# Kernel tuning notes

Hardware: AMD Instinct MI355X
Metric: run time of the kernel (lower is better)

The kernel has to match this reference:

```python
import jax, jax.numpy as jnp
import numpy as np

D = 1024; NH = 16; HD = D // NH; B = 2; L = 2048
BASE_FAST = (1.0 + 5.0 ** 0.5) / 2.0
BASE_SLOW = 1618.0
BASE_GLU = 16180.0
ALPHA_ATTN = 0.42; ALPHA_MLP = 1.07; ALPHA_ADV = 1.0
H_GATE = max(8, D // 4)   # rope_gate hidden
H_NU = max(4, D // 8)     # DuplexViscosity hidden
LN_EPS = 1e-5


def _rope_cos_sin(seq_len, dim, base, dtype=jnp.float32):
    idx = jnp.arange(0, dim, 2, dtype=dtype) / float(dim)
    inv = 1.0 / (base ** idx)
    t = jnp.arange(seq_len, dtype=dtype)
    freqs = jnp.outer(t, inv)                       # (L, D/2)
    emb = jnp.concatenate([freqs, freqs], axis=-1)  # (L, D)
    return jnp.cos(emb)[None], jnp.sin(emb)[None]   # (1, L, D)


def _rotate_half(x):
    x1, x2 = jnp.split(x, 2, axis=-1)
    return jnp.concatenate([-x2, x1], axis=-1)


def _apply_rope(x, cos, sin):
    return x * cos + _rotate_half(x) * sin


def setup_inputs() -> dict:
    key = jax.random.key(0)
    ks = jax.random.split(key, 16)
    std = 0.02
    # all Linear weights stored as (in, out) so forward is x @ W + b
    return {
        "z": jax.random.normal(ks[0], (B, L, D), jnp.float32),
        "Wq": jax.random.normal(ks[1], (D, D), jnp.float32) * std,
        "bq": jnp.zeros((D,), jnp.float32),
        "Wk": jax.random.normal(ks[2], (D, D), jnp.float32) * std,
        "bk": jnp.zeros((D,), jnp.float32),
        "Wv": jax.random.normal(ks[3], (D, D), jnp.float32) * std,
        "bv": jnp.zeros((D,), jnp.float32),
        "Wcoh": jax.random.normal(ks[4], (D, D), jnp.float32) * std,
        "gamma": jnp.zeros((1,), jnp.float32),
        "rg_w1": jax.random.normal(ks[5], (D, H_GATE), jnp.float32) * std,
        "rg_b1": jnp.zeros((H_GATE,), jnp.float32),
        "rg_w2": jax.random.normal(ks[6], (H_GATE, 1), jnp.float32) * std,
        "rg_b2": jnp.zeros((1,), jnp.float32),
        "nu_diff": jnp.asarray(0.2, jnp.float32),
        "nu_adv": jnp.asarray(0.01, jnp.float32),
        "nu_w1": jax.random.normal(ks[7], (D, H_NU), jnp.float32) * std,
        "nu_b1": jnp.zeros((H_NU,), jnp.float32),
        "nu_w2": jax.random.normal(ks[8], (H_NU, 1), jnp.float32) * std,
        "nu_b2": jnp.zeros((1,), jnp.float32),
        "Wu": jax.random.normal(ks[9], (D, D), jnp.float32) * std,
        "bu": jnp.zeros((D,), jnp.float32),
        "Wg": jax.random.normal(ks[10], (D, D), jnp.float32) * std,
        "bg": jnp.zeros((D,), jnp.float32),
        "ln_w": jnp.ones((D,), jnp.float32),
        "ln_b": jnp.zeros((D,), jnp.float32),
        "Cw": jax.random.normal(ks[11], (D, D), jnp.float32) * std,
        "Cb": jnp.zeros((D,), jnp.float32),
    }


def reference(z, Wq, bq, Wk, bk, Wv, bv, Wcoh, gamma, rg_w1, rg_b1, rg_w2, rg_b2,
              nu_diff, nu_adv, nu_w1, nu_b1, nu_w2, nu_b2, Wu, bu, Wg, bg,
              ln_w, ln_b, Cw, Cb):
    b, l, d = z.shape
    dt = z.dtype
    # causal cumulative mean pool[t] = mean(z[0..t])
    pool = jnp.cumsum(z, axis=1) / jnp.arange(1, l + 1, dtype=dt)[None, :, None]

    # QKV projections
    Q = z @ Wq + bq
    K_raw = z @ Wk + bk
    V = z @ Wv + bv

    # global coherence bias: (B, Lq, Lk)
    gk = pool @ Wcoh
    gb = jnp.einsum('bld,bmd->blm', gk, K_raw) * (d ** -0.5)
    gb = jnp.tanh(gamma[0]) * gb

    # hybrid RoPE gate (small MLP on pool, exact gelu as in torch)
    gate = jax.nn.sigmoid(jax.nn.gelu(pool @ rg_w1 + rg_b1, approximate=False) @ rg_w2 + rg_b2)  # (B,L,1)
    cos_f, sin_f = _rope_cos_sin(l, d, BASE_FAST, dt)
    cos_s, sin_s = _rope_cos_sin(l, d, BASE_SLOW, dt)
    cos = gate * cos_f + (1.0 - gate) * cos_s
    sin = gate * sin_f + (1.0 - gate) * sin_s
    Qr = _apply_rope(Q, cos, sin)
    Kr = _apply_rope(K_raw, cos, sin)

    # multi-head causal attention with fused coherence bias
    Qh = Qr.reshape(b, l, NH, HD).transpose(0, 2, 1, 3)
    Kh = Kr.reshape(b, l, NH, HD).transpose(0, 2, 1, 3)
    Vh = V.reshape(b, l, NH, HD).transpose(0, 2, 1, 3)
    logits = jnp.einsum('bhld,bhmd->bhlm', Qh, Kh) * (HD ** -0.5)
    logits = logits + gb[:, None]
    causal = jnp.tril(jnp.ones((l, l), bool))
    logits = jnp.where(causal[None, None], logits, -jnp.inf)
    attn = jax.nn.softmax(logits, axis=-1)
    attn_out = jnp.einsum('bhlm,bhmd->bhld', attn, Vh).transpose(0, 2, 1, 3).reshape(b, l, d)
    attn_w = attn.mean(axis=1)

    # DuplexViscosity on causal pool
    delta = jnp.tanh(jnp.tanh(pool @ nu_w1 + nu_b1) @ nu_w2 + nu_b2) * jnp.abs(nu_adv)
    nu_b = jnp.abs(nu_diff) + delta  # (B,L,1)

    # GLU branch with fixed slow-base RoPE
    cos_g, sin_g = _rope_cos_sin(l, d, BASE_GLU, dt)
    z_glu = _apply_rope(z, cos_g, sin_g)
    bilinear = (z_glu @ Wu + bu) * (z_glu @ Wg + bg)
    adv = -(ALPHA_ADV * nu_b) * bilinear
    mu = adv.mean(axis=-1, keepdims=True)
    var = ((adv - mu) ** 2).mean(axis=-1, keepdims=True)
    adv_n = (adv - mu) * jax.lax.rsqrt(var + LN_EPS) * ln_w + ln_b
    mlp_out = adv_n @ Cw + Cb

    z_next = z + ALPHA_ATTN * attn_out + ALPHA_MLP * mlp_out
    return z_next, attn_w
```

## Files before the change

kernel.cpp:

```cpp
#include <hip/hip_runtime.h>

#define DD 1024
#define NHH 16
#define HDD 64
#define BB 2
#define LL 2048
#define MM (BB*LL)
#define HG 256
#define HN 128

#define LOG_FAST 0.48121182f
#define LOG_SLOW 7.3889461f
#define LOG_GLU  9.6915312f
#define SCL 0.18033688f

typedef __attribute__((ext_vector_type(8))) short short8;
typedef __attribute__((ext_vector_type(4))) float f32x4;

__device__ __forceinline__ float gelu_f(float x) {
    return 0.5f * x * (1.0f + erff(x * 0.70710678f));
}

__device__ __forceinline__ ushort f2b(float x) {
    unsigned u = __float_as_uint(x);
    unsigned r = (u + 0x7FFFu + ((u >> 16) & 1u)) >> 16;
    return (ushort)r;
}

__device__ __forceinline__ float b2f(ushort x) {
    return __uint_as_float(((unsigned)x) << 16);
}

__device__ __forceinline__ void gl_lds16(const ushort* g, ushort* l) {
    __builtin_amdgcn_global_load_lds(
        (const __attribute__((address_space(1))) unsigned int*)g,
        (__attribute__((address_space(3))) unsigned int*)l, 16, 0, 0);
}

#define SWZC(row, c8) (((((row) << 3) | ((c8) ^ ((row) & 7)))) << 3)

__device__ __forceinline__ void stage_tile(const ushort* gsrc, int rstride,
                                           ushort* lds, int tid) {
    int wid = tid >> 6;
#pragma unroll
    for (int r = 0; r < 2; ++r) {
        int c = r * 256 + tid;
        int row = c >> 3;
        int c8 = (c & 7) ^ (row & 7);
        gl_lds16(gsrc + (size_t)row * rstride + c8 * 8,
                 lds + (size_t)(r * 256 + wid * 64) * 8);
    }
}

#define LCH 128
#define NCH 16
__global__ void pool_scan1(const float* __restrict__ z, float* __restrict__ part,
                           float* __restrict__ ctot, ushort* __restrict__ zb) {
    int ch = blockIdx.x, dg = blockIdx.y, b = blockIdx.z;
    int d = dg * 256 + threadIdx.x;
    size_t base = ((size_t)b * LL + ch * LCH) * DD + d;
    const float* zp = z + base;
    float* pp = part + base;
    ushort* zo = zb + base;
    float s = 0.f;
    for (int t = 0; t < LCH; ++t) {
        float v = zp[(size_t)t * DD];
        s += v;
        pp[(size_t)t * DD] = s;
        zo[(size_t)t * DD] = f2b(v);
    }
    ctot[((size_t)b * NCH + ch) * DD + d] = s;
}
__global__ void pool_scan2(const float* __restrict__ part, const float* __restrict__ ctot,
                           ushort* __restrict__ poolb) {
    int ch = blockIdx.x, dg = blockIdx.y, b = blockIdx.z;
    int d = dg * 256 + threadIdx.x;
    float off = 0.f;
    for (int c = 0; c < ch; ++c) off += ctot[((size_t)b * NCH + c) * DD + d];
    int t0 = ch * LCH;
    size_t base = ((size_t)b * LL + t0) * DD + d;
    const float* pp = part + base;
    ushort* po = poolb + base;
    for (int t = 0; t < LCH; ++t) {
        po[(size_t)t * DD] = f2b((pp[(size_t)t * DD] + off) / (float)(t0 + t + 1));
    }
}

__global__ void f2bT4_kernel(const float* __restrict__ W0, const float* __restrict__ W1,
                             const float* __restrict__ W2, const float* __restrict__ W3,
                             ushort* __restrict__ Wt) {
    const float* W = blockIdx.z == 0 ? W0 : (blockIdx.z == 1 ? W1 :
                     (blockIdx.z == 2 ? W2 : W3));
    ushort* dst = Wt + (size_t)blockIdx.z * 1024 * 1024;
    __shared__ float t[32][33];
    int n0 = blockIdx.x * 32, k0 = blockIdx.y * 32;
    int tx = threadIdx.x & 31, ty = threadIdx.x >> 5;
#pragma unroll
    for (int j = 0; j < 4; ++j)
        t[ty + j * 8][tx] = W[(size_t)(k0 + ty + j * 8) * 1024 + n0 + tx];
    __syncthreads();
#pragma unroll
    for (int j = 0; j < 4; ++j)
        dst[(size_t)(n0 + ty + j * 8) * 1024 + k0 + tx] = f2b(t[tx][ty + j * 8]);
}

__global__ void f2bT_rgnu(const float* __restrict__ Wrg, const float* __restrict__ Wnu,
                          ushort* __restrict__ WtRG, ushort* __restrict__ WtNU) {
    int zc = blockIdx.z;
    if (zc == 1 && blockIdx.x >= 4) return;
    const float* W = zc == 0 ? Wrg : Wnu;
    ushort* dst = zc == 0 ? WtRG : WtNU;
    int Ndim = zc == 0 ? HG : HN;
    __shared__ float t[32][33];
    int n0 = blockIdx.x * 32, k0 = blockIdx.y * 32;
    int tx = threadIdx.x & 31, ty = threadIdx.x >> 5;
#pragma unroll
    for (int j = 0; j < 4; ++j)
        t[ty + j * 8][tx] = W[(size_t)(k0 + ty + j * 8) * Ndim + n0 + tx];
    __syncthreads();
#pragma unroll
    for (int j = 0; j < 4; ++j)
        dst[(size_t)(n0 + ty + j * 8) * 1024 + k0 + tx] = f2b(t[tx][ty + j * 8]);
}

__global__ void f2bT3_kernel(const float* __restrict__ W0, const float* __restrict__ W1,
                             const float* __restrict__ W2, ushort* __restrict__ Wt) {
    const float* W = blockIdx.z == 0 ? W0 : (blockIdx.z == 1 ? W1 : W2);
    ushort* dst = Wt + (size_t)blockIdx.z * 1024 * 1024;
    __shared__ float t[32][33];
    int n0 = blockIdx.x * 32, k0 = blockIdx.y * 32;
    int tx = threadIdx.x & 31, ty = threadIdx.x >> 5;
#pragma unroll
    for (int j = 0; j < 4; ++j)
        t[ty + j * 8][tx] = W[(size_t)(k0 + ty + j * 8) * 1024 + n0 + tx];
    __syncthreads();
#pragma unroll
    for (int j = 0; j < 4; ++j)
        dst[(size_t)(n0 + ty + j * 8) * 1024 + k0 + tx] = f2b(t[tx][ty + j * 8]);
}

__global__ __launch_bounds__(256) void gemm_mfma(
        const ushort* __restrict__ A, const ushort* __restrict__ Wt,
        const float* __restrict__ bias, float* __restrict__ C, int Ndim) {
    __shared__ ushort As[4096];
    __shared__ ushort Bs[4096];
    int tid = threadIdx.x;
    int wid = tid >> 6, lane = tid & 63;
    int n0 = blockIdx.x * 128, m0 = blockIdx.y * 128;
    int wm = wid >> 1, wn = wid & 1;
    int quad = lane >> 4, l16 = lane & 15;

    f32x4 acc[4][4];
#pragma unroll
    for (int mi = 0; mi < 4; ++mi)
#pragma unroll
        for (int ni = 0; ni < 4; ++ni) acc[mi][ni] = (f32x4){0.f, 0.f, 0.f, 0.f};

    int c0 = wid * 128 + lane;
    int c1 = c0 + 64;
    const ushort* Ag0 = A + (size_t)(m0 + (c0 & 127)) * 1024 + (c0 >> 7) * 8;
    const ushort* Ag1 = A + (size_t)(m0 + (c1 & 127)) * 1024 + (c1 >> 7) * 8;
    const ushort* Bg0 = Wt + (size_t)(n0 + (c0 & 127)) * 1024 + (c0 >> 7) * 8;
    const ushort* Bg1 = Wt + (size_t)(n0 + (c1 & 127)) * 1024 + (c1 >> 7) * 8;
    ushort* Al0 = As + wid * 1024;
    ushort* Al1 = As + wid * 1024 + 512;
    ushort* Bl0 = Bs + wid * 1024;
    ushort* Bl1 = Bs + wid * 1024 + 512;

    const ushort* a_rd = &As[(quad * 128 + wm * 64 + l16) * 8];
    const ushort* b_rd = &Bs[(quad * 128 + wn * 64 + l16) * 8];

    for (int kb = 0; kb < 1024; kb += 32) {
        gl_lds16(Ag0 + kb, Al0);
        gl_lds16(Ag1 + kb, Al1);
        gl_lds16(Bg0 + kb, Bl0);
        gl_lds16(Bg1 + kb, Bl1);
        __syncthreads();
        short8 af[4], bf[4];
#pragma unroll
        for (int mi = 0; mi < 4; ++mi)
            af[mi] = *(const short8*)(a_rd + mi * 16 * 8);
#pragma unroll
        for (int ni = 0; ni < 4; ++ni)
            bf[ni] = *(const short8*)(b_rd + ni * 16 * 8);
#pragma unroll
        for (int mi = 0; mi < 4; ++mi)
#pragma unroll
            for (int ni = 0; ni < 4; ++ni)
                acc[mi][ni] = __builtin_amdgcn_mfma_f32_16x16x32_bf16(
                    af[mi], bf[ni], acc[mi][ni], 0, 0, 0);
        __syncthreads();
    }
    int bcol[4];
    float bval[4];
#pragma unroll
    for (int ni = 0; ni < 4; ++ni) {
        bcol[ni] = n0 + wn * 64 + ni * 16 + l16;
        bval[ni] = bias ? bias[bcol[ni]] : 0.f;
    }
#pragma unroll
    for (int mi = 0; mi < 4; ++mi) {
#pragma unroll
        for (int r = 0; r < 4; ++r) {
            int row = m0 + wm * 64 + mi * 16 + quad * 4 + r;
            float* Cp = C + (size_t)row * Ndim;
#pragma unroll
            for (int ni = 0; ni < 4; ++ni)
                Cp[bcol[ni]] = acc[mi][ni][r] + bval[ni];
        }
    }
}

__global__ __launch_bounds__(256) void gemm_mfma3(
        const ushort* __restrict__ A, const ushort* __restrict__ Wt,
        const float* __restrict__ b0, const float* __restrict__ b1,
        const float* __restrict__ b2, float* __restrict__ C,
        ushort* __restrict__ K16r) {
    int zid = blockIdx.z;
    const ushort* W = Wt + (size_t)zid * 1024 * 1024;
    const float* bias = zid == 0 ? b0 : (zid == 1 ? b1 : b2);
    float* Cz = C + (size_t)zid * (size_t)MM * DD;
    __shared__ ushort As[4096];
    __shared__ ushort Bs[4096];
    int tid = threadIdx.x;
    int wid = tid >> 6, lane = tid & 63;
    int n0 = blockIdx.x * 128, m0 = blockIdx.y * 128;
    int wm = wid >> 1, wn = wid & 1;
    int quad = lane >> 4, l16 = lane & 15;

    f32x4 acc[4][4];
#pragma unroll
    for (int mi = 0; mi < 4; ++mi)
#pragma unroll
        for (int ni = 0; ni < 4; ++ni) acc[mi][ni] = (f32x4){0.f, 0.f, 0.f, 0.f};

    int c0 = wid * 128 + lane;
    int c1 = c0 + 64;
    const ushort* Ag0 = A + (size_t)(m0 + (c0 & 127)) * 1024 + (c0 >> 7) * 8;
    const ushort* Ag1 = A + (size_t)(m0 + (c1 & 127)) * 1024 + (c1 >> 7) * 8;
    const ushort* Bg0 = W + (size_t)(n0 + (c0 & 127)) * 1024 + (c0 >> 7) * 8;
    const ushort* Bg1 = W + (size_t)(n0 + (c1 & 127)) * 1024 + (c1 >> 7) * 8;
    ushort* Al0 = As + wid * 1024;
    ushort* Al1 = As + wid * 1024 + 512;
    ushort* Bl0 = Bs + wid * 1024;
    ushort* Bl1 = Bs + wid * 1024 + 512;

    const ushort* a_rd = &As[(quad * 128 + wm * 64 + l16) * 8];
    const ushort* b_rd = &Bs[(quad * 128 + wn * 64 + l16) * 8];

    for (int kb = 0; kb < 1024; kb += 32) {
        gl_lds16(Ag0 + kb, Al0);
        gl_lds16(Ag1 + kb, Al1);
        gl_lds16(Bg0 + kb, Bl0);
        gl_lds16(Bg1 + kb, Bl1);
        __syncthreads();
        short8 af[4], bf[4];
#pragma unroll
        for (int mi = 0; mi < 4; ++mi)
            af[mi] = *(const short8*)(a_rd + mi * 16 * 8);
#pragma unroll
        for (int ni = 0; ni < 4; ++ni)
            bf[ni] = *(const short8*)(b_rd + ni * 16 * 8);
#pragma unroll
        for (int mi = 0; mi < 4; ++mi)
#pragma unroll
            for (int ni = 0; ni < 4; ++ni)
                acc[mi][ni] = __builtin_amdgcn_mfma_f32_16x16x32_bf16(
                    af[mi], bf[ni], acc[mi][ni], 0, 0, 0);
        __syncthreads();
    }
    float bval[4];
    int bcol[4];
#pragma unroll
    for (int ni = 0; ni < 4; ++ni) {
        bcol[ni] = n0 + wn * 64 + ni * 16 + l16;
        bval[ni] = bias[bcol[ni]];
    }
    bool doK = (zid == 1) && (K16r != nullptr);
#pragma unroll
    for (int mi = 0; mi < 4; ++mi) {
#pragma unroll
        for (int r = 0; r < 4; ++r) {
            int row = m0 + wm * 64 + mi * 16 + quad * 4 + r;
            float* Cp = Cz + (size_t)row * 1024;
            ushort* Kp = K16r + (size_t)row * 1024;
#pragma unroll
            for (int ni = 0; ni < 4; ++ni) {
                float v = acc[mi][ni][r] + bval[ni];
                Cp[bcol[ni]] = v;
                if (doK) Kp[bcol[ni]] = f2b(v);
            }
        }
    }
}

__global__ __launch_bounds__(256) void gemm_mfma_b16out(
        const ushort* __restrict__ A, const ushort* __restrict__ Wt,
        ushort* __restrict__ C, int Ndim) {
    __shared__ ushort As[4096];
    __shared__ ushort Bs[4096];
    int tid = threadIdx.x;
    int wid = tid >> 6, lane = tid & 63;
    int n0 = blockIdx.x * 128, m0 = blockIdx.y * 128;
    int wm = wid >> 1, wn = wid & 1;
    int quad = lane >> 4, l16 = lane & 15;

    f32x4 acc[4][4];
#pragma unroll
    for (int mi = 0; mi < 4; ++mi)
#pragma unroll
        for (int ni = 0; ni < 4; ++ni) acc[mi][ni] = (f32x4){0.f, 0.f, 0.f, 0.f};

    int c0 = wid * 128 + lane;
    int c1 = c0 + 64;
    const ushort* Ag0 = A + (size_t)(m0 + (c0 & 127)) * 1024 + (c0 >> 7) * 8;
    const ushort* Ag1 = A + (size_t)(m0 + (c1 & 127)) * 1024 + (c1 >> 7) * 8;
    const ushort* Bg0 = Wt + (size_t)(n0 + (c0 & 127)) * 1024 + (c0 >> 7) * 8;
    const ushort* Bg1 = Wt + (size_t)(n0 + (c1 & 127)) * 1024 + (c1 >> 7) * 8;
    ushort* Al0 = As + wid * 1024;
    ushort* Al1 = As + wid * 1024 + 512;
    ushort* Bl0 = Bs + wid * 1024;
    ushort* Bl1 = Bs + wid * 1024 + 512;

    const ushort* a_rd = &As[(quad * 128 + wm * 64 + l16) * 8];
    const ushort* b_rd = &Bs[(quad * 128 + wn * 64 + l16) * 8];

    for (int kb = 0; kb < 1024; kb += 32) {
        gl_lds16(Ag0 + kb, Al0);
        gl_lds16(Ag1 + kb, Al1);
        gl_lds16(Bg0 + kb, Bl0);
        gl_lds16(Bg1 + kb, Bl1);
        __syncthreads();
        short8 af[4], bf[4];
#pragma unroll
        for (int mi = 0; mi < 4; ++mi)
            af[mi] = *(const short8*)(a_rd + mi * 16 * 8);
#pragma unroll
        for (int ni = 0; ni < 4; ++ni)
            bf[ni] = *(const short8*)(b_rd + ni * 16 * 8);
#pragma unroll
        for (int mi = 0; mi < 4; ++mi)
#pragma unroll
            for (int ni = 0; ni < 4; ++ni)
                acc[mi][ni] = __builtin_amdgcn_mfma_f32_16x16x32_bf16(
                    af[mi], bf[ni], acc[mi][ni], 0, 0, 0);
        __syncthreads();
    }
#pragma unroll
    for (int mi = 0; mi < 4; ++mi) {
#pragma unroll
        for (int r = 0; r < 4; ++r) {
            int row = m0 + wm * 64 + mi * 16 + quad * 4 + r;
            ushort* Cp = C + (size_t)row * Ndim;
#pragma unroll
            for (int ni = 0; ni < 4; ++ni)
                Cp[n0 + wn * 64 + ni * 16 + l16] = f2b(acc[mi][ni][r]);
        }
    }
}

__global__ __launch_bounds__(256) void gemm_gates(
        const ushort* __restrict__ A, const ushort* __restrict__ WtRG,
        const ushort* __restrict__ WtNU, const float* __restrict__ rg_b1,
        const float* __restrict__ nu_b1, float* __restrict__ H1,
        float* __restrict__ N1) {
    int bx = blockIdx.x;
    bool isH = bx < 2;
    const ushort* Wt = isH ? WtRG : WtNU;
    const float* bias = isH ? rg_b1 : nu_b1;
    float* C = isH ? H1 : N1;
    int Ndim = isH ? HG : HN;
    int n0 = isH ? bx * 128 : 0;
    int m0 = blockIdx.y * 128;
    __shared__ ushort As[4096];
    __shared__ ushort Bs[4096];
    int tid = threadIdx.x;
    int wid = tid >> 6, lane = tid & 63;
    int wm = wid >> 1, wn = wid & 1;
    int quad = lane >> 4, l16 = lane & 15;

    f32x4 acc[4][4];
#pragma unroll
    for (int mi = 0; mi < 4; ++mi)
#pragma unroll
        for (int ni = 0; ni < 4; ++ni) acc[mi][ni] = (f32x4){0.f, 0.f, 0.f, 0.f};

    int c0 = wid * 128 + lane;
    int c1 = c0 + 64;
    const ushort* Ag0 = A + (size_t)(m0 + (c0 & 127)) * 1024 + (c0 >> 7) * 8;
    const ushort* Ag1 = A + (size_t)(m0 + (c1 & 127)) * 1024 + (c1 >> 7) * 8;
    const ushort* Bg0 = Wt + (size_t)(n0 + (c0 & 127)) * 1024 + (c0 >> 7) * 8;
    const ushort* Bg1 = Wt + (size_t)(n0 + (c1 & 127)) * 1024 + (c1 >> 7) * 8;
    ushort* Al0 = As + wid * 1024;
    ushort* Al1 = As + wid * 1024 + 512;
    ushort* Bl0 = Bs + wid * 1024;
    ushort* Bl1 = Bs + wid * 1024 + 512;

    const ushort* a_rd = &As[(quad * 128 + wm * 64 + l16) * 8];
    const ushort* b_rd = &Bs[(quad * 128 + wn * 64 + l16) * 8];

    for (int kb = 0; kb < 1024; kb += 32) {
        gl_lds16(Ag0 + kb, Al0);
        gl_lds16(Ag1 + kb, Al1);
        gl_lds16(Bg0 + kb, Bl0);
        gl_lds16(Bg1 + kb, Bl1);
        __syncthreads();
        short8 af[4], bf[4];
#pragma unroll
        for (int mi = 0; mi < 4; ++mi)
            af[mi] = *(const short8*)(a_rd + mi * 16 * 8);
#pragma unroll
        for (int ni = 0; ni < 4; ++ni)
            bf[ni] = *(const short8*)(b_rd + ni * 16 * 8);
#pragma unroll
        for (int mi = 0; mi < 4; ++mi)
#pragma unroll
            for (int ni = 0; ni < 4; ++ni)
                acc[mi][ni] = __builtin_amdgcn_mfma_f32_16x16x32_bf16(
                    af[mi], bf[ni], acc[mi][ni], 0, 0, 0);
        __syncthreads();
    }
    int bcol[4];
    float bval[4];
#pragma unroll
    for (int ni = 0; ni < 4; ++ni) {
        bcol[ni] = n0 + wn * 64 + ni * 16 + l16;
        bval[ni] = bias[bcol[ni]];
    }
#pragma unroll
    for (int mi = 0; mi < 4; ++mi) {
#pragma unroll
        for (int r = 0; r < 4; ++r) {
            int row = m0 + wm * 64 + mi * 16 + quad * 4 + r;
            float* Cp = C + (size_t)row * Ndim;
#pragma unroll
            for (int ni = 0; ni < 4; ++ni)
                Cp[bcol[ni]] = acc[mi][ni][r] + bval[ni];
        }
    }
}

__global__ __launch_bounds__(256) void gb_mfma(
        const ushort* __restrict__ gk16, const ushort* __restrict__ K16r,
        const float* __restrict__ gamma, ushort* __restrict__ gb) {
    int lt = blockIdx.x >> 4, mt = blockIdx.x & 15;
    if (mt > lt) return;
    int b = blockIdx.y;
    __shared__ ushort As[4096];
    __shared__ ushort Bs[4096];
    int tid = threadIdx.x;
    int wid = tid >> 6, lane = tid & 63;
    int l0 = lt * 128, m0 = mt * 128;
    int wm = wid >> 1, wn = wid & 1;
    int quad = lane >> 4, l16 = lane & 15;

    f32x4 acc[4][4];
#pragma unroll
    for (int mi = 0; mi < 4; ++mi)
#pragma unroll
        for (int ni = 0; ni < 4; ++ni) acc[mi][ni] = (f32x4){0.f, 0.f, 0.f, 0.f};

    int c0 = wid * 128 + lane;
    int c1 = c0 + 64;
    const ushort* Ag0 = gk16 + ((size_t)b * LL + l0 + (c0 & 127)) * 1024 + (c0 >> 7) * 8;
    const ushort* Ag1 = gk16 + ((size_t)b * LL + l0 + (c1 & 127)) * 1024 + (c1 >> 7) * 8;
    const ushort* Bg0 = K16r + ((size_t)b * LL + m0 + (c0 & 127)) * 1024 + (c0 >> 7) * 8;
    const ushort* Bg1 = K16r + ((size_t)b * LL + m0 + (c1 & 127)) * 1024 + (c1 >> 7) * 8;
    ushort* Al0 = As + wid * 1024;
    ushort* Al1 = As + wid * 1024 + 512;
    ushort* Bl0 = Bs + wid * 1024;
    ushort* Bl1 = Bs + wid * 1024 + 512;

    const ushort* a_rd = &As[(quad * 128 + wm * 64 + l16) * 8];
    const ushort* b_rd = &Bs[(quad * 128 + wn * 64 + l16) * 8];

    for (int kb = 0; kb < 1024; kb += 32) {
        gl_lds16(Ag0 + kb, Al0);
        gl_lds16(Ag1 + kb, Al1);
        gl_lds16(Bg0 + kb, Bl0);
        gl_lds16(Bg1 + kb, Bl1);
        __syncthreads();
        short8 af[4], bf[4];
#pragma unroll
        for (int mi = 0; mi < 4; ++mi)
            af[mi] = *(const short8*)(a_rd + mi * 16 * 8);
#pragma unroll
        for (int ni = 0; ni < 4; ++ni)
            bf[ni] = *(const short8*)(b_rd + ni * 16 * 8);
#pragma unroll
        for (int mi = 0; mi < 4; ++mi)
#pragma unroll
            for (int ni = 0; ni < 4; ++ni)
                acc[mi][ni] = __builtin_amdgcn_mfma_f32_16x16x32_bf16(
                    af[mi], bf[ni], acc[mi][ni], 0, 0, 0);
        __syncthreads();
    }
    float scale = tanhf(gamma[0]) * 0.25f;
#pragma unroll
    for (int mi = 0; mi < 4; ++mi) {
#pragma unroll
        for (int r = 0; r < 4; ++r) {
            int row = l0 + wm * 64 + mi * 16 + quad * 4 + r;
            ushort* Cp = gb + ((size_t)b * LL + row) * LL;
            ushort4 o;
            o.x = f2b(acc[mi][0][r] * scale);
            o.y = f2b(acc[mi][1][r] * scale);
            o.z = f2b(acc[mi][2][r] * scale);
            o.w = f2b(acc[mi][3][r] * scale);
            *(ushort4*)(Cp + m0 + wn * 64 + l16 * 4) = o;
        }
    }
}

__global__ __launch_bounds__(256) void gatenu_fin(
        const float* __restrict__ H1, const float* __restrict__ N1,
        const float* __restrict__ rg_w2, const float* __restrict__ rg_b2,
        const float* __restrict__ nu_w2, const float* __restrict__ nu_b2,
        const float* __restrict__ nu_diff, const float* __restrict__ nu_adv,
        float* __restrict__ gate, float* __restrict__ nub) {
    int row = blockIdx.x, tid = threadIdx.x;
    float gv = gelu_f(H1[(size_t)row * HG + tid]) * rg_w2[tid];
    float nv = (tid < HN) ? tanhf(N1[(size_t)row * HN + tid]) * nu_w2[tid] : 0.f;
    for (int off = 32; off; off >>= 1) {
        gv += __shfl_down(gv, off);
        nv += __shfl_down(nv, off);
    }
    __shared__ float pg[4], pn[4];
    if ((tid & 63) == 0) { pg[tid >> 6] = gv; pn[tid >> 6] = nv; }
    __syncthreads();
    if (tid == 0) {
        float ga = pg[0] + pg[1] + pg[2] + pg[3] + rg_b2[0];
        gate[row] = 1.f / (1.f + expf(-ga));
        float na = pn[0] + pn[1] + pn[2] + pn[3] + nu_b2[0];
        nub[row] = fabsf(nu_diff[0]) + tanhf(na) * fabsf(nu_adv[0]);
    }
}

__global__ void rope_qk_bf16(const float* __restrict__ Q, const float* __restrict__ K,
                             const float* __restrict__ gate,
                             ushort* __restrict__ Q16, ushort* __restrict__ K16) {
    int idx = blockIdx.x * 256 + threadIdx.x;
    int row = idx >> 9;
    int i = idx & 511;
    int b = row >> 11, t = row & (LL - 1);
    float g = gate[row];
    float fi = (float)i * (1.0f / 512.0f);
    float tf = (float)t;
    float af = tf * expf(-fi * LOG_FAST);
    float as = tf * expf(-fi * LOG_SLOW);
    float c = g * cosf(af) + (1.f - g) * cosf(as);
    float s = g * sinf(af) + (1.f - g) * sinf(as);
    size_t base = (size_t)row * DD;
    float x = Q[base + i], y = Q[base + 512 + i];
    float q1 = x * c - y * s, q2 = y * c + x * s;
    x = K[base + i]; y = K[base + 512 + i];
    float k1 = x * c - y * s, k2 = y * c + x * s;
    int h1 = i >> 6, d1 = i & 63;
    size_t o1 = ((size_t)(b * 16 + h1) * LL + t) * 64 + d1;
    size_t o2 = ((size_t)(b * 16 + 8 + h1) * LL + t) * 64 + d1;
    Q16[o1] = f2b(q1); Q16[o2] = f2b(q2);
    K16[o1] = f2b(k1); K16[o2] = f2b(k2);
}

__global__ __launch_bounds__(256) void vt16_kernel(const float* __restrict__ V,
                                                   ushort* __restrict__ VT) {
    __shared__ ushort t[64][72];
    int lb = blockIdx.x, hb = blockIdx.y, b = blockIdx.z;
    int tid = threadIdx.x;
    {
        int l = tid >> 2, c0 = (tid & 3) * 16;
        const float* Vp = V + ((size_t)(b * LL) + lb * 64 + l) * DD + hb * 64 + c0;
#pragma unroll
        for (int j = 0; j < 4; ++j) {
            float4 v = *(const float4*)(Vp + j * 4);
            t[l][c0 + j * 4 + 0] = f2b(v.x);
            t[l][c0 + j * 4 + 1] = f2b(v.y);
            t[l][c0 + j * 4 + 2] = f2b(v.z);
            t[l][c0 + j * 4 + 3] = f2b(v.w);
        }
    }
    __syncthreads();
    {
        int d = tid >> 2, l0 = (tid & 3) * 16;
        ushort tmp[16];
#pragma unroll
        for (int j = 0; j < 16; ++j) tmp[j] = t[l0 + j][d];
        ushort* Op = VT + ((size_t)((b * 16 + hb) * 64) + d) * LL + lb * 64 + l0;
        *(ushort4*)(Op + 0)  = *(ushort4*)&tmp[0];
        *(ushort4*)(Op + 4)  = *(ushort4*)&tmp[4];
        *(ushort4*)(Op + 8)  = *(ushort4*)&tmp[8];
        *(ushort4*)(Op + 12) = *(ushort4*)&tmp[12];
    }
}

__global__ void rope_glu_b16(const float* __restrict__ z, ushort* __restrict__ zg) {
    int idx = blockIdx.x * 256 + threadIdx.x;
    int row = idx >> 9;
    int i = idx & 511;
    int t = row & (LL - 1);
    float fi = (float)i * (1.0f / 512.0f);
    float ag = (float)t * expf(-fi * LOG_GLU);
    float c = cosf(ag), s = sinf(ag);
    size_t base = (size_t)row * DD;
    float x = z[base + i], y = z[base + 512 + i];
    zg[base + i]       = f2b(x * c - y * s);
    zg[base + 512 + i] = f2b(y * c + x * s);
}

__global__ __launch_bounds__(256, 4) void attn_flash_mfma(
        const ushort* __restrict__ Q16, const ushort* __restrict__ K16,
        const ushort* __restrict__ VT16, const ushort* __restrict__ gb16,
        float* __restrict__ attn_out, float* __restrict__ stats) {
    int h = blockIdx.x, qt = 31 - blockIdx.y, b = blockIdx.z;
    __shared__ ushort Ks0[4096];
    __shared__ ushort Vs0[4096];
    __shared__ ushort Ks1[4096];
    __shared__ ushort Vs1[4096];
    __shared__ ushort Ps[4096];
    int tid = threadIdx.x, wid = tid >> 6, lane = tid & 63;
    int quad = lane >> 4, l16 = lane & 15;
    const ushort* Qg = Q16 + ((size_t)(b * 16 + h) * LL) * 64;
    const ushort* Kg = K16 + ((size_t)(b * 16 + h) * LL) * 64;
    const ushort* Vg = VT16 + ((size_t)(b * 16 + h) * 64) * LL;
    const ushort* gbB = gb16 + (size_t)b * LL * LL;
    float* stB = stats + ((size_t)(b * 16 + h) * LL) * 2;
    int qrow = wid * 16 + quad * 4;
    int q0 = qt * 64;

    short8 qf[2];
    {
        const ushort* qp = Qg + (size_t)(q0 + wid * 16 + l16) * 64 + quad * 8;
        qf[0] = *(const short8*)(qp);
        qf[1] = *(const short8*)(qp + 32);
    }
    stage_tile(Kg, 64, Ks0, tid);
    stage_tile(Vg, LL, Vs0, tid);
    __syncthreads();

    ushort* Pw = Ps + wid * 1024;

    short ov = (l16 == 0) ? (short)0x3F80 : (short)0;
    short8 onesf = {ov, ov, ov, ov, ov, ov, ov, ov};

    f32x4 ofr[5];
    float m_r[4];
#pragma unroll
    for (int nt = 0; nt < 5; ++nt) ofr[nt] = (f32x4){0.f, 0.f, 0.f, 0.f};
#pragma unroll
    for (int r = 0; r < 4; ++r) m_r[r] = -3e38f;

#define FLASH_PHASE(KC, VC, KN, VN, T) do {                                       \
    int k0_ = (T) * 64;                                                           \
    ushort4 gw_[4];                                                               \
    _Pragma("unroll")                                                             \
    for (int r = 0; r < 4; ++r)                                                   \
        gw_[r] = *(const ushort4*)(gbB + (size_t)(q0 + qrow + r) * LL + k0_ + l16 * 4); \
    f32x4 sf_[4];                                                                 \
    _Pragma("unroll")                                                             \
    for (int nt = 0; nt < 4; ++nt) sf_[nt] = (f32x4){0.f, 0.f, 0.f, 0.f};         \
    _Pragma("unroll")                                                             \
    for (int ks = 0; ks < 2; ++ks)                                                \
        _Pragma("unroll")                                                         \
        for (int nt = 0; nt < 4; ++nt) {                                          \
            short8 kf_ = *(const short8*)((KC) + SWZC(nt * 16 + l16, ks * 4 + quad)); \
            sf_[nt] = __builtin_amdgcn_mfma_f32_16x16x32_bf16(qf[ks], kf_, sf_[nt], 0, 0, 0); \
        }                                                                         \
    short8 vf_[2][4];                                                             \
    _Pragma("unroll")                                                             \
    for (int ks = 0; ks < 2; ++ks)                                                \
        _Pragma("unroll")                                                         \
        for (int nt = 0; nt < 4; ++nt)                                            \
            vf_[ks][nt] = *(const short8*)((VC) + SWZC(nt * 16 + l16, ks * 4 + quad)); \
    if ((T) + 1 <= qt) {                                                          \
        stage_tile(Kg + (size_t)(k0_ + 64) * 64, 64, (KN), tid);                  \
        stage_tile(Vg + (k0_ + 64), LL, (VN), tid);                               \
    }                                                                             \
    _Pragma("unroll")                                                             \
    for (int r = 0; r < 4; ++r) {                                                 \
        sf_[0][r] += b2f(gw_[r].x); sf_[1][r] += b2f(gw_[r].y);                   \
        sf_[2][r] += b2f(gw_[r].z); sf_[3][r] += b2f(gw_[r].w);                   \
    }                                                                             \
    if ((T) == qt) {                                                              \
        _Pragma("unroll")                                                         \
        for (int nt = 0; nt < 4; ++nt)                                            \
            _Pragma("unroll")                                                     \
            for (int r = 0; r < 4; ++r)                                           \
                if (nt * 16 + l16 > qrow + r) sf_[nt][r] = -1e30f;                \
    }                                                                             \
    float alpha_[4], mS_[4];                                                      \
    _Pragma("unroll")                                                             \
    for (int r = 0; r < 4; ++r) {                                                 \
        float m_ = fmaxf(fmaxf(sf_[0][r], sf_[1][r]), fmaxf(sf_[2][r], sf_[3][r])); \
        _Pragma("unroll")                                                         \
        for (int off = 1; off < 16; off <<= 1)                                    \
            m_ = fmaxf(m_, __shfl_xor(m_, off));                                  \
        float nm_ = fmaxf(m_r[r], m_);                                            \
        alpha_[r] = __builtin_amdgcn_exp2f((m_r[r] - nm_) * SCL);                 \
        m_r[r] = nm_;                                                             \
        mS_[r] = nm_ * SCL;                                                       \
    }                                                                             \
    _Pragma("unroll")                                                             \
    for (int nt = 0; nt < 4; ++nt)                                                \
        _Pragma("unroll")                                                         \
        for (int r = 0; r < 4; ++r) {                                             \
            float p_ = __builtin_amdgcn_exp2f(fmaf(sf_[nt][r], SCL, -mS_[r]));    \
            int prow_ = quad * 4 + r;                                             \
            int chk_ = (nt * 2) | (l16 >> 3);                                     \
            Pw[prow_ * 64 + ((chk_ ^ (prow_ & 7)) << 3) + (l16 & 7)] = f2b(p_);   \
        }                                                                         \
    _Pragma("unroll")                                                             \
    for (int nt = 0; nt < 5; ++nt)                                                \
        _Pragma("unroll")                                                         \
        for (int r = 0; r < 4; ++r) ofr[nt][r] *= alpha_[r];                      \
    short8 pf_[2];                                                                \
    _Pragma("unroll")                                                             \
    for (int ks = 0; ks < 2; ++ks)                                                \
        pf_[ks] = *(const short8*)(Pw + l16 * 64 + (((ks * 4 + quad) ^ (l16 & 7)) << 3)); \
    __builtin_amdgcn_s_setprio(1);                                                \
    _Pragma("unroll")                                                             \
    for (int ks = 0; ks < 2; ++ks) {                                              \
        _Pragma("unroll")                                                         \
        for (int nt = 0; nt < 4; ++nt)                                            \
            ofr[nt] = __builtin_amdgcn_mfma_f32_16x16x32_bf16(pf_[ks], vf_[ks][nt], ofr[nt], 0, 0, 0); \
        ofr[4] = __builtin_amdgcn_mfma_f32_16x16x32_bf16(pf_[ks], onesf, ofr[4], 0, 0, 0); \
    }                                                                             \
    __builtin_amdgcn_s_setprio(0);                                                \
    __syncthreads();                                                              \
} while (0)

    for (int kt = 0; kt <= qt; kt += 2) {
        FLASH_PHASE(Ks0, Vs0, Ks1, Vs1, kt);
        if (kt + 1 <= qt) FLASH_PHASE(Ks1, Vs1, Ks0, Vs0, kt + 1);
    }
#undef FLASH_PHASE

#pragma unroll
    for (int r = 0; r < 4; ++r) {
        float l = __shfl(ofr[4][r], (lane & 48));
        float rinv = 1.0f / l;
        float* op = attn_out + ((size_t)(b * LL) + q0 + qrow + r) * DD + h * 64 + l16;
#pragma unroll
        for (int nt = 0; nt < 4; ++nt)
            op[nt * 16] = ofr[nt][r] * rinv;
    }
    if (l16 == 0) {
#pragma unroll
        for (int r = 0; r < 4; ++r) {
            size_t si = (size_t)(q0 + qrow + r) * 2;
            stB[si]     = m_r[r];
            stB[si + 1] = ofr[4][r];
        }
    }
}

__global__ __launch_bounds__(256, 4) void attn_w_mfma(
        const ushort* __restrict__ Q16, const ushort* __restrict__ K16,
        const ushort* __restrict__ gb16, const float* __restrict__ stats,
        float* __restrict__ aw) {
    int qt = blockIdx.x >> 5, kt = blockIdx.x & 31;
    int b = blockIdx.y;
    int tid = threadIdx.x, wid = tid >> 6, lane = tid & 63;
    int quad = lane >> 4, l16 = lane & 15;
    int q0 = qt * 64, k0 = kt * 64;
    int qrow = wid * 16 + quad * 4;
    if (kt > qt) {
        int rr = tid >> 2, c0 = (tid & 3) * 16;
        float4 zv = make_float4(0.f, 0.f, 0.f, 0.f);
        float* p = aw + ((size_t)(b * LL) + q0 + rr) * LL + k0 + c0;
#pragma unroll
        for (int j = 0; j < 4; ++j) *(float4*)(p + j * 4) = zv;
        return;
    }
    __shared__ ushort Qs0[4096];
    __shared__ ushort Ks0[4096];
    __shared__ ushort Qs1[4096];
    __shared__ ushort Ks1[4096];
    float acc[4][4];
#pragma unroll
    for (int nt = 0; nt < 4; ++nt)
#pragma unroll
        for (int r = 0; r < 4; ++r) acc[nt][r] = 0.f;
    f32x4 gacc[4];
    const ushort* gbB = gb16 + (size_t)b * LL * LL;
#pragma unroll
    for (int r = 0; r < 4; ++r) {
        ushort4 g4 = *(const ushort4*)(gbB + (size_t)(q0 + qrow + r) * LL + k0 + l16 * 4);
        gacc[0][r] = b2f(g4.x);
        gacc[1][r] = b2f(g4.y);
        gacc[2][r] = b2f(g4.z);
        gacc[3][r] = b2f(g4.w);
    }
    bool diag = (kt == qt);
    stage_tile(Q16 + ((size_t)(b * 16) * LL + q0) * 64, 64, Qs0, tid);
    stage_tile(K16 + ((size_t)(b * 16) * LL + k0) * 64, 64, Ks0, tid);
    __syncthreads();

#define AW_PHASE(QC, KC, QN, KN, H) do {                                          \
    short8 qf_[2], kf_[2][4];                                                     \
    _Pragma("unroll")                                                             \
    for (int ks = 0; ks < 2; ++ks)                                                \
        qf_[ks] = *(const short8*)((QC) + SWZC(wid * 16 + l16, ks * 4 + quad));   \
    _Pragma("unroll")                                                             \
    for (int ks = 0; ks < 2; ++ks)                                                \
        _Pragma("unroll")                                                         \
        for (int nt = 0; nt < 4; ++nt)                                            \
            kf_[ks][nt] = *(const short8*)((KC) + SWZC(nt * 16 + l16, ks * 4 + quad)); \
    if ((H) < 15) {                                                               \
        stage_tile(Q16 + ((size_t)(b * 16 + (H) + 1) * LL + q0) * 64, 64, (QN), tid); \
        stage_tile(K16 + ((size_t)(b * 16 + (H) + 1) * LL + k0) * 64, 64, (KN), tid); \
    }                                                                             \
    float mS_[4], li_[4];                                                         \
    {                                                                             \
        const float* sp_ = stats + ((size_t)(b * 16 + (H)) * LL + q0 + qrow) * 2; \
        _Pragma("unroll")                                                         \
        for (int r = 0; r < 4; ++r) {                                             \
            mS_[r] = sp_[r * 2] * SCL;                                            \
            li_[r] = 1.0f / sp_[r * 2 + 1];                                       \
        }                                                                         \
    }                                                                             \
    f32x4 sf_[4];                                                                 \
    _Pragma("unroll")                                                             \
    for (int nt = 0; nt < 4; ++nt) sf_[nt] = gacc[nt];                            \
    __builtin_amdgcn_s_setprio(1);                                                \
    _Pragma("unroll")                                                             \
    for (int ks = 0; ks < 2; ++ks)                                                \
        _Pragma("unroll")                                                         \
        for (int nt = 0; nt < 4; ++nt)                                            \
            sf_[nt] = __builtin_amdgcn_mfma_f32_16x16x32_bf16(qf_[ks], kf_[ks][nt], sf_[nt], 0, 0, 0); \
    __builtin_amdgcn_s_setprio(0);                                                \
    _Pragma("unroll")                                                             \
    for (int nt = 0; nt < 4; ++nt)                                                \
        _Pragma("unroll")                                                         \
        for (int r = 0; r < 4; ++r) {                                             \
            int row_ = qrow + r;                                                  \
            if (!diag || (nt * 16 + l16 <= row_))                                 \
                acc[nt][r] += __builtin_amdgcn_exp2f(fmaf(sf_[nt][r], SCL, -mS_[r])) * li_[r]; \
        }                                                                         \
    __syncthreads();                                                              \
} while (0)

    for (int h = 0; h < NHH; h += 2) {
        AW_PHASE(Qs0, Ks0, Qs1, Ks1, h);
        AW_PHASE(Qs1, Ks1, Qs0, Ks0, h + 1);
    }
#undef AW_PHASE

#pragma unroll
    for (int r = 0; r < 4; ++r) {
        float* op = aw + ((size_t)(b * LL) + q0 + qrow + r) * LL + k0 + l16;
#pragma unroll
        for (int nt = 0; nt < 4; ++nt)
            op[nt * 16] = acc[nt][r] * 0.0625f;
    }
}

__global__ __launch_bounds__(256) void adv_ln_kernel(
        const float* __restrict__ U, const float* __restrict__ G,
        const float* __restrict__ nub, const float* __restrict__ lnw,
        const float* __restrict__ lnb, ushort* __restrict__ out) {
    int row = blockIdx.x, tid = threadIdx.x;
    size_t base = (size_t)row * DD + tid * 4;
    float4 u4 = *(const float4*)&U[base];
    float4 g4 = *(const float4*)&G[base];
    float nu = nub[row];
    float a[4];
    a[0] = -nu * u4.x * g4.x;
    a[1] = -nu * u4.y * g4.y;
    a[2] = -nu * u4.z * g4.z;
    a[3] = -nu * u4.w * g4.w;
    float ts = a[0] + a[1] + a[2] + a[3];
    float tq = a[0] * a[0] + a[1] * a[1] + a[2] * a[2] + a[3] * a[3];
    for (int off = 32; off; off >>= 1) {
        ts += __shfl_down(ts, off);
        tq += __shfl_down(tq, off);
    }
    __shared__ float r1[4], r2[4];
    if ((tid & 63) == 0) { r1[tid >> 6] = ts; r2[tid >> 6] = tq; }
    __syncthreads();
    __shared__ float s_mu, s_rs;
    if (tid == 0) {
        float S  = r1[0] + r1[1] + r1[2] + r1[3];
        float Qq = r2[0] + r2[1] + r2[2] + r2[3];
        float mu = S * (1.0f / 1024.f);
        float var = Qq * (1.0f / 1024.f) - mu * mu;
        s_mu = mu;
        s_rs = rsqrtf(var + 1e-5f);
    }
    __syncthreads();
    float mu = s_mu, rs = s_rs;
    float4 w4 = *(const float4*)&lnw[tid * 4];
    float4 b4 = *(const float4*)&lnb[tid * 4];
    ushort4 ov;
    ov.x = f2b((a[0] - mu) * rs * w4.x + b4.x);
    ov.y = f2b((a[1] - mu) * rs * w4.y + b4.y);
    ov.z = f2b((a[2] - mu) * rs * w4.z + b4.z);
    ov.w = f2b((a[3] - mu) * rs * w4.w + b4.w);
    *(ushort4*)&out[base] = ov;
}

__global__ void final_kernel(const float* __restrict__ z, const float* __restrict__ ao,
                             const float* __restrict__ mlp, float* __restrict__ out) {
    size_t i = ((size_t)blockIdx.x * 256 + threadIdx.x) * 4;
    float4 z4 = *(const float4*)&z[i];
    float4 a4 = *(const float4*)&ao[i];
    float4 m4 = *(const float4*)&mlp[i];
    float4 o;
    o.x = z4.x + 0.42f * a4.x + 1.07f * m4.x;
    o.y = z4.y + 0.42f * a4.y + 1.07f * m4.y;
    o.z = z4.z + 0.42f * a4.z + 1.07f * m4.z;
    o.w = z4.w + 0.42f * a4.w + 1.07f * m4.w;
    *(float4*)&out[i] = o;
}

extern "C" void kernel_launch(void* const* d_in, const int* in_sizes, int n_in,
                              void* d_out, int out_size, void* d_ws, size_t ws_size,
                              hipStream_t stream) {
    const float* z       = (const float*)d_in[0];
    const float* Wq      = (const float*)d_in[1];
    const float* bq      = (const float*)d_in[2];
    const float* Wk      = (const float*)d_in[3];
    const float* bk      = (const float*)d_in[4];
    const float* Wv      = (const float*)d_in[5];
    const float* bv      = (const float*)d_in[6];
    const float* Wcoh    = (const float*)d_in[7];
    const float* gamma   = (const float*)d_in[8];
    const float* rg_w1   = (const float*)d_in[9];
    const float* rg_b1   = (const float*)d_in[10];
    const float* rg_w2   = (const float*)d_in[11];
    const float* rg_b2   = (const float*)d_in[12];
    const float* nu_diff = (const float*)d_in[13];
    const float* nu_adv  = (const float*)d_in[14];
    const float* nu_w1   = (const float*)d_in[15];
    const float* nu_b1   = (const float*)d_in[16];
    const float* nu_w2   = (const float*)d_in[17];
    const float* nu_b2   = (const float*)d_in[18];
    const float* Wu      = (const float*)d_in[19];
    const float* bu      = (const float*)d_in[20];
    const float* Wg      = (const float*)d_in[21];
    const float* bg      = (const float*)d_in[22];
    const float* ln_w    = (const float*)d_in[23];
    const float* ln_b    = (const float*)d_in[24];
    const float* Cw      = (const float*)d_in[25];
    const float* Cb      = (const float*)d_in[26];

    float* out_z  = (float*)d_out;
    float* out_aw = out_z + (size_t)MM * DD;

    float* ws = (float*)d_ws;
    const size_t MD = (size_t)MM * DD;
    float* pool  = ws;
    float* Qb    = ws + MD;
    float* Kb    = ws + 2 * MD;
    float* Vb    = ws + 3 * MD;
    float* gkb   = ws + 4 * MD;
    float* gbb   = ws + 5 * MD;
    float* H1    = ws + 7 * MD;
    float* N1    = H1 + (size_t)MM * HG;
    float* gate  = N1 + (size_t)MM * HN;
    float* nub   = gate + MM;
    float* stats = nub + MM;
    float* ctot  = stats + (size_t)BB * NHH * LL * 2;

    char* gbase  = (char*)gbb;
    ushort* Ab   = (ushort*)gbase;
    ushort* Wb   = (ushort*)(gbase + (size_t)8 * 1024 * 1024);
    ushort* gb16 = (ushort*)(gbase + (size_t)16 * 1024 * 1024);
    ushort* WtRG = Wb;
    ushort* WtNU = Wb + (size_t)1024 * 1024;
    ushort* Q16  = (ushort*)Vb;
    ushort* K16  = (ushort*)Vb + MD;
    ushort* VT16 = (ushort*)pool;
    ushort* poolb = (ushort*)pool;
    float*  part = gkb;
    ushort* gk16 = (ushort*)gkb;
    ushort* K16r = (ushort*)gkb + MD;

    dim3 g128(8, 32);
    dim3 wT_g(32, 32);

    pool_scan1<<<dim3(NCH, 4, BB), 256, 0, stream>>>(z, part, ctot, Ab);
    pool_scan2<<<dim3(NCH, 4, BB), 256, 0, stream>>>(part, ctot, poolb);
    f2bT4_kernel<<<dim3(32, 32, 4), 256, 0, stream>>>(Wq, Wk, Wv, Wcoh, Wb);
    gemm_mfma3<<<dim3(8, 32, 3), 256, 0, stream>>>(Ab, Wb, bq, bk, bv, Qb, K16r);
    gemm_mfma_b16out<<<g128, 256, 0, stream>>>(poolb, Wb + (size_t)3 * 1024 * 1024, gk16, DD);
    f2bT_rgnu<<<dim3(8, 32, 2), 256, 0, stream>>>(rg_w1, nu_w1, WtRG, WtNU);
    gemm_gates<<<dim3(3, 32), 256, 0, stream>>>(poolb, WtRG, WtNU, rg_b1, nu_b1, H1, N1);
    gb_mfma<<<dim3(256, BB), 256, 0, stream>>>(gk16, K16r, gamma, gb16);
    gatenu_fin<<<dim3(MM), 256, 0, stream>>>(H1, N1, rg_w2, rg_b2, nu_w2, nu_b2,
                                             nu_diff, nu_adv, gate, nub);
    vt16_kernel<<<dim3(32, 16, BB), 256, 0, stream>>>(Vb, VT16);
    rope_qk_bf16<<<dim3((MM * 512) / 256), 256, 0, stream>>>(Qb, Kb, gate, Q16, K16);
    attn_flash_mfma<<<dim3(NHH, 32, BB), 256, 0, stream>>>(Q16, K16, VT16, gb16, gkb, stats);
    attn_w_mfma<<<dim3(1024, BB), 256, 0, stream>>>(Q16, K16, gb16, stats, out_aw);
    rope_glu_b16<<<dim3((MM * 512) / 256), 256, 0, stream>>>(z, Ab);
    f2bT3_kernel<<<dim3(32, 32, 3), 256, 0, stream>>>(Wu, Wg, Cw, Wb);
    gemm_mfma3<<<dim3(8, 32, 2), 256, 0, stream>>>(Ab, Wb, bu, bg, bg, Qb, nullptr);
    adv_ln_kernel<<<dim3(MM), 256, 0, stream>>>(Qb, Kb, nub, ln_w, ln_b, Ab);
    gemm_mfma<<<g128, 256, 0, stream>>>(Ab, Wb + (size_t)2 * 1024 * 1024, Cb, Qb, DD);
    final_kernel<<<dim3(MD / 4 / 256), 256, 0, stream>>>(z, gkb, Qb, out_z);
}
```

Measured before the change: 654.2 us.

## Pair causal query tiles per block and reorder fragment loads in attention

Each flash-attention block now handles two query tiles, qt and 31-qt, in sequence. This balances the causal workload across blocks and halves the grid, with launch bounds relaxed from 4 to 2 blocks per SM. The K/V prefetch is moved ahead of the QK MFMAs, the bias is loaded straight into the accumulators, and V and K fragments are read from LDS just before use instead of being preloaded. These changes cut register pressure and give the prefetch more time to complete, at the cost of fewer blocks in flight for latency hiding.

Measured after the change: 565.1 us. -13.6%, faster.

```diff
diff --git a/kernel.cpp b/kernel.cpp
--- a/kernel.cpp
+++ b/kernel.cpp
@@ -607,11 +607,11 @@
     zg[base + 512 + i] = f2b(y * c + x * s);
 }
 
-__global__ __launch_bounds__(256, 4) void attn_flash_mfma(
+__global__ __launch_bounds__(256, 2) void attn_flash_mfma(
         const ushort* __restrict__ Q16, const ushort* __restrict__ K16,
         const ushort* __restrict__ VT16, const ushort* __restrict__ gb16,
         float* __restrict__ attn_out, float* __restrict__ stats) {
-    int h = blockIdx.x, qt = 31 - blockIdx.y, b = blockIdx.z;
+    int h = blockIdx.x, b = blockIdx.z;
     __shared__ ushort Ks0[4096];
     __shared__ ushort Vs0[4096];
     __shared__ ushort Ks1[4096];
@@ -625,39 +625,24 @@
     const ushort* gbB = gb16 + (size_t)b * LL * LL;
     float* stB = stats + ((size_t)(b * 16 + h) * LL) * 2;
     int qrow = wid * 16 + quad * 4;
-    int q0 = qt * 64;
-
-    short8 qf[2];
-    {
-        const ushort* qp = Qg + (size_t)(q0 + wid * 16 + l16) * 64 + quad * 8;
-        qf[0] = *(const short8*)(qp);
-        qf[1] = *(const short8*)(qp + 32);
-    }
-    stage_tile(Kg, 64, Ks0, tid);
-    stage_tile(Vg, LL, Vs0, tid);
-    __syncthreads();
-
     ushort* Pw = Ps + wid * 1024;
 
     short ov = (l16 == 0) ? (short)0x3F80 : (short)0;
     short8 onesf = {ov, ov, ov, ov, ov, ov, ov, ov};
 
-    f32x4 ofr[5];
-    float m_r[4];
-#pragma unroll
-    for (int nt = 0; nt < 5; ++nt) ofr[nt] = (f32x4){0.f, 0.f, 0.f, 0.f};
-#pragma unroll
-    for (int r = 0; r < 4; ++r) m_r[r] = -3e38f;
-
 #define FLASH_PHASE(KC, VC, KN, VN, T) do {                                       \
     int k0_ = (T) * 64;                                                           \
-    ushort4 gw_[4];                                                               \
-    _Pragma("unroll")                                                             \
-    for (int r = 0; r < 4; ++r)                                                   \
-        gw_[r] = *(const ushort4*)(gbB + (size_t)(q0 + qrow + r) * LL + k0_ + l16 * 4); \
+    if ((T) + 1 <= qt) {                                                          \
+        stage_tile(Kg + (size_t)(k0_ + 64) * 64, 64, (KN), tid);                  \
+        stage_tile(Vg + (k0_ + 64), LL, (VN), tid);                               \
+    }                                                                             \
     f32x4 sf_[4];                                                                 \
     _Pragma("unroll")                                                             \
-    for (int nt = 0; nt < 4; ++nt) sf_[nt] = (f32x4){0.f, 0.f, 0.f, 0.f};         \
+    for (int r = 0; r < 4; ++r) {                                                 \
+        ushort4 g4_ = *(const ushort4*)(gbB + (size_t)(q0 + qrow + r) * LL + k0_ + l16 * 4); \
+        sf_[0][r] = b2f(g4_.x); sf_[1][r] = b2f(g4_.y);                           \
+        sf_[2][r] = b2f(g4_.z); sf_[3][r] = b2f(g4_.w);                           \
+    }                                                                             \
     _Pragma("unroll")                                                             \
     for (int ks = 0; ks < 2; ++ks)                                                \
         _Pragma("unroll")                                                         \
@@ -665,21 +650,6 @@
             short8 kf_ = *(const short8*)((KC) + SWZC(nt * 16 + l16, ks * 4 + quad)); \
             sf_[nt] = __builtin_amdgcn_mfma_f32_16x16x32_bf16(qf[ks], kf_, sf_[nt], 0, 0, 0); \
         }                                                                         \
-    short8 vf_[2][4];                                                             \
-    _Pragma("unroll")                                                             \
-    for (int ks = 0; ks < 2; ++ks)                                                \
-        _Pragma("unroll")                                                         \
-        for (int nt = 0; nt < 4; ++nt)                                            \
-            vf_[ks][nt] = *(const short8*)((VC) + SWZC(nt * 16 + l16, ks * 4 + quad)); \
-    if ((T) + 1 <= qt) {                                                          \
-        stage_tile(Kg + (size_t)(k0_ + 64) * 64, 64, (KN), tid);                  \
-        stage_tile(Vg + (k0_ + 64), LL, (VN), tid);                               \
-    }                                                                             \
-    _Pragma("unroll")                                                             \
-    for (int r = 0; r < 4; ++r) {                                                 \
-        sf_[0][r] += b2f(gw_[r].x); sf_[1][r] += b2f(gw_[r].y);                   \
-        sf_[2][r] += b2f(gw_[r].z); sf_[3][r] += b2f(gw_[r].w);                   \
-    }                                                                             \
     if ((T) == qt) {                                                              \
         _Pragma("unroll")                                                         \
         for (int nt = 0; nt < 4; ++nt)                                            \
@@ -720,37 +690,62 @@
     _Pragma("unroll")                                                             \
     for (int ks = 0; ks < 2; ++ks) {                                              \
         _Pragma("unroll")                                                         \
-        for (int nt = 0; nt < 4; ++nt)                                            \
-            ofr[nt] = __builtin_amdgcn_mfma_f32_16x16x32_bf16(pf_[ks], vf_[ks][nt], ofr[nt], 0, 0, 0); \
+        for (int nt = 0; nt < 4; ++nt) {                                          \
+            short8 vf_ = *(const short8*)((VC) + SWZC(nt * 16 + l16, ks * 4 + quad)); \
+            ofr[nt] = __builtin_amdgcn_mfma_f32_16x16x32_bf16(pf_[ks], vf_, ofr[nt], 0, 0, 0); \
+        }                                                                         \
         ofr[4] = __builtin_amdgcn_mfma_f32_16x16x32_bf16(pf_[ks], onesf, ofr[4], 0, 0, 0); \
     }                                                                             \
     __builtin_amdgcn_s_setprio(0);                                                \
     __syncthreads();                                                              \
 } while (0)
 
-    for (int kt = 0; kt <= qt; kt += 2) {
-        FLASH_PHASE(Ks0, Vs0, Ks1, Vs1, kt);
-        if (kt + 1 <= qt) FLASH_PHASE(Ks1, Vs1, Ks0, Vs0, kt + 1);
+#pragma unroll 1
+    for (int sel = 0; sel < 2; ++sel) {
+        int qt = sel ? (31 - (int)blockIdx.y) : (int)blockIdx.y;
+        int q0 = qt * 64;
+
+        short8 qf[2];
+        {
+            const ushort* qp = Qg + (size_t)(q0 + wid * 16 + l16) * 64 + quad * 8;
+            qf[0] = *(const short8*)(qp);
+            qf[1] = *(const short8*)(qp + 32);
+        }
+        stage_tile(Kg, 64, Ks0, tid);
+        stage_tile(Vg, LL, Vs0, tid);
+        __syncthreads();
+
+        f32x4 ofr[5];
+        float m_r[4];
+#pragma unroll
+        for (int nt = 0; nt < 5; ++nt) ofr[nt] = (f32x4){0.f, 0.f, 0.f, 0.f};
+#pragma unroll
+        for (int r = 0; r < 4; ++r) m_r[r] = -3e38f;
+
+        for (int kt = 0; kt <= qt; kt += 2) {
+            FLASH_PHASE(Ks0, Vs0, Ks1, Vs1, kt);
+            if (kt + 1 <= qt) FLASH_PHASE(Ks1, Vs1, Ks0, Vs0, kt + 1);
+        }
+
+#pragma unroll
+        for (int r = 0; r < 4; ++r) {
+            float l = __shfl(ofr[4][r], (lane & 48));
+            float rinv = 1.0f / l;
+            float* op = attn_out + ((size_t)(b * LL) + q0 + qrow + r) * DD + h * 64 + l16;
+#pragma unroll
+            for (int nt = 0; nt < 4; ++nt)
+                op[nt * 16] = ofr[nt][r] * rinv;
+        }
+        if (l16 == 0) {
+#pragma unroll
+            for (int r = 0; r < 4; ++r) {
+                size_t si = (size_t)(q0 + qrow + r) * 2;
+                stB[si]     = m_r[r];
+                stB[si + 1] = ofr[4][r];
+            }
+        }
     }
 #undef FLASH_PHASE
-
-#pragma unroll
-    for (int r = 0; r < 4; ++r) {
-        float l = __shfl(ofr[4][r], (lane & 48));
-        float rinv = 1.0f / l;
-        float* op = attn_out + ((size_t)(b * LL) + q0 + qrow + r) * DD + h * 64 + l16;
-#pragma unroll
-        for (int nt = 0; nt < 4; ++nt)
-            op[nt * 16] = ofr[nt][r] * rinv;
-    }
-    if (l16 == 0) {
-#pragma unroll
-        for (int r = 0; r < 4; ++r) {
-            size_t si = (size_t)(q0 + qrow + r) * 2;
-            stB[si]     = m_r[r];
-            stB[si + 1] = ofr[4][r];
-        }
-    }
 }
 
 __global__ __launch_bounds__(256, 4) void attn_w_mfma(
@@ -796,19 +791,14 @@
     __syncthreads();
 
 #define AW_PHASE(QC, KC, QN, KN, H) do {                                          \
-    short8 qf_[2], kf_[2][4];                                                     \
-    _Pragma("unroll")                                                             \
-    for (int ks = 0; ks < 2; ++ks)                                                \
-        qf_[ks] = *(const short8*)((QC) + SWZC(wid * 16 + l16, ks * 4 + quad));   \
-    _Pragma("unroll")                                                             \
-    for (int ks = 0; ks < 2; ++ks)                                                \
-        _Pragma("unroll")                                                         \
-        for (int nt = 0; nt < 4; ++nt)                                            \
-            kf_[ks][nt] = *(const short8*)((KC) + SWZC(nt * 16 + l16, ks * 4 + quad)); \
     if ((H) < 15) {                                                               \
         stage_tile(Q16 + ((size_t)(b * 16 + (H) + 1) * LL + q0) * 64, 64, (QN), tid); \
         stage_tile(K16 + ((size_t)(b * 16 + (H) + 1) * LL + k0) * 64, 64, (KN), tid); \
     }                                                                             \
+    short8 qf_[2];                                                                \
+    _Pragma("unroll")                                                             \
+    for (int ks = 0; ks < 2; ++ks)                                                \
+        qf_[ks] = *(const short8*)((QC) + SWZC(wid * 16 + l16, ks * 4 + quad));   \
     float mS_[4], li_[4];                                                         \
     {                                                                             \
         const float* sp_ = stats + ((size_t)(b * 16 + (H)) * LL + q0 + qrow) * 2; \
@@ -825,8 +815,10 @@
     _Pragma("unroll")                                                             \
     for (int ks = 0; ks < 2; ++ks)                                                \
         _Pragma("unroll")                                                         \
-        for (int nt = 0; nt < 4; ++nt)                                            \
-            sf_[nt] = __builtin_amdgcn_mfma_f32_16x16x32_bf16(qf_[ks], kf_[ks][nt], sf_[nt], 0, 0, 0); \
+        for (int nt = 0; nt < 4; ++nt) {                                          \
+            short8 kf_ = *(const short8*)((KC) + SWZC(nt * 16 + l16, ks * 4 + quad)); \
+            sf_[nt] = __builtin_amdgcn_mfma_f32_16x16x32_bf16(qf_[ks], kf_, sf_[nt], 0, 0, 0); \
+        }                                                                         \
     __builtin_amdgcn_s_setprio(0);                                                \
     _Pragma("unroll")                                                             \
     for (int nt = 0; nt < 4; ++nt)                                                \
@@ -990,7 +982,7 @@
                                              nu_diff, nu_adv, gate, nub);
     vt16_kernel<<<dim3(32, 16, BB), 256, 0, stream>>>(Vb, VT16);
     rope_qk_bf16<<<dim3((MM * 512) / 256), 256, 0, stream>>>(Qb, Kb, gate, Q16, K16);
-    attn_flash_mfma<<<dim3(NHH, 32, BB), 256, 0, stream>>>(Q16, K16, VT16, gb16, gkb, stats);
+    attn_flash_mfma<<<dim3(NHH, 16, BB), 256, 0, stream>>>(Q16, K16, VT16, gb16, gkb, stats);
     attn_w_mfma<<<dim3(1024, BB), 256, 0, stream>>>(Q16, K16, gb16, stats, out_aw);
     rope_glu_b16<<<dim3((MM * 512) / 256), 256, 0, stream>>>(z, Ab);
     f2bT3_kernel<<<dim3(32, 32, 3), 256, 0, stream>>>(Wu, Wg, Cw, Wb);
```
